# Optimization experiments

Hardware: AMD Instinct MI355X
Metric: run time of the kernel (lower is better)

Reference implementation:

```python
import jax, jax.numpy as jnp
import numpy as np

TEMPERATURE = 0.8
TOP_K = 50
TOP_P = 0.9
REP_PENALTY = 1.2
FILTER_VALUE = -1e9  # stands in for -inf in HF top_k_top_p_filtering (numerically identical probs)

B, S, V = 16, 64, 50257
P = 64  # previously generated tokens per sequence


def setup_inputs() -> dict:
    key = jax.random.key(0)
    k1, k2 = jax.random.split(key)
    logits = jax.random.normal(k1, (B, S, V), dtype=jnp.float32) * 3.0
    prev_tokens = jax.random.randint(k2, (S, P), 0, V)
    return {"logits": logits, "prev_tokens": prev_tokens}


def _repetition_penalty(logits, prev_tokens):
    # logits: [B,S,V], prev_tokens: [S,P]
    gathered = jnp.take_along_axis(logits, prev_tokens[None, :, :], axis=-1)  # [B,S,P]
    all_neg = jnp.all(gathered < 0, axis=0, keepdims=True)                    # [1,S,P]
    penalized = jnp.where(all_neg, gathered * REP_PENALTY, gathered / REP_PENALTY)
    s_idx = jnp.broadcast_to(jnp.arange(S)[:, None], prev_tokens.shape)       # [S,P]
    # scatter back (duplicate indices write identical values -> matches set() semantics)
    return logits.at[:, s_idx, prev_tokens].set(penalized)


def _top_k_top_p_filter(logits):
    # top-k: mask everything below the k-th largest logit
    if TOP_K > 0:
        kth = jax.lax.top_k(logits, TOP_K)[0][..., -1:]                       # [B,S,1]
        logits = jnp.where(logits < kth, FILTER_VALUE, logits)
    # top-p (nucleus): sort descending, mask tokens past cumulative prob TOP_P
    if TOP_P < 1.0:
        sort_idx = jnp.argsort(-logits, axis=-1)                              # [B,S,V]
        sorted_logits = jnp.take_along_axis(logits, sort_idx, axis=-1)
        cum_probs = jnp.cumsum(jax.nn.softmax(sorted_logits, axis=-1), axis=-1)
        remove_sorted = cum_probs > TOP_P
        # shift right so the first token exceeding the threshold is kept
        remove_sorted = jnp.concatenate(
            [jnp.zeros_like(remove_sorted[..., :1]), remove_sorted[..., :-1]], axis=-1)
        inv_idx = jnp.argsort(sort_idx, axis=-1)
        remove = jnp.take_along_axis(remove_sorted, inv_idx, axis=-1)
        logits = jnp.where(remove, FILTER_VALUE, logits)
    return logits


def reference(logits, prev_tokens):
    if REP_PENALTY != 1.0:
        logits = _repetition_penalty(logits, prev_tokens)
    logits = logits / TEMPERATURE
    logits = _top_k_top_p_filter(logits)
    # Categorical(logits=...) normalizes logits; return normalized log-probs
    return jax.nn.log_softmax(logits, axis=-1)
```

## Files before the change

kernel.cpp:

```cpp
#include <hip/hip_runtime.h>
#include <cstdint>
#include <cfloat>
#include <math.h>

#define BB 16
#define SS 64
#define VV 50257
#define PP 64

#define NT 1024
#define HNT 512
#define NBLK 512
#define BINS 2048
#define CAP 1536
#define BMW 1572
#define KCAP 128
#define BCAP 512
#define TRAW 6.0f

typedef float f32x4 __attribute__((ext_vector_type(4)));

__device__ __forceinline__ uint32_t fkey(float f) {
    uint32_t u = __float_as_uint(f);
    return u ^ ((uint32_t)((int32_t)u >> 31) | 0x80000000u);
}
__device__ __forceinline__ float key2f(uint32_t u) {
    uint32_t b = (u & 0x80000000u) ? (u ^ 0x80000000u) : ~u;
    return __uint_as_float(b);
}

__global__ __launch_bounds__(NT)
void sch_kernel(const float* __restrict__ logits,
                const int* __restrict__ prev,
                float* __restrict__ out)
{
    const int g   = blockIdx.x;
    const int rA  = g;
    const int rB  = g + NBLK;
    const int s   = g % SS;
    const int bA  = rA / SS;
    const int bB  = rB / SS;
    const int tid = threadIdx.x;
    const float* rowA  = logits + (size_t)rA * VV;
    const float* rowB  = logits + (size_t)rB * VV;
    float*       orowA = out    + (size_t)rA * VV;
    float*       orowB = out    + (size_t)rB * VV;

    __shared__ uint32_t s_bm[BMW];
    __shared__ float    s_cv[CAP];
    __shared__ int      s_ci[CAP];
    __shared__ float    s_cv2[CAP];
    __shared__ int      s_ci2[CAP];
    __shared__ uint32_t s_hist[BINS];
    __shared__ uint32_t s_scan[16];
    __shared__ int      s_ptok[PP];
    __shared__ int      s_pneg[PP];
    __shared__ float    s_prawA[PP];
    __shared__ float    s_prawB[PP];
    __shared__ float    s_ppenA[PP];
    __shared__ float    s_ppenB[PP];
    __shared__ float    s_binv[BCAP];
    __shared__ double   s_v64[KCAP];
    __shared__ double   s_e64[KCAP];
    __shared__ int      s_ki[KCAP];
    __shared__ float    s_kof[KCAP];
    __shared__ int      s_kiA[KCAP];
    __shared__ float    s_kofA[KCAP];
    __shared__ int    s_cnt, s_cnt2, s_cntinv, s_b50, s_need, s_cntb, s_k50, s_kp, s_Kk;
    __shared__ int    s_hbar;
    __shared__ float  s_kth, s_rc;
    __shared__ double s_lse;

    for (int i = tid; i < BMW; i += NT) s_bm[i] = 0u;
    if (tid < PP) s_pneg[tid] = 1;
    if (tid == 0) { s_cnt = 0; s_cnt2 = 0; s_cntinv = 0; s_hbar = 0; }
    __syncthreads();
    for (int pair = tid; pair < PP * BB; pair += NT) {
        int ti = pair & (PP - 1);
        int b2 = pair >> 6;
        int tok = prev[s * PP + ti];
        float gg = logits[((size_t)b2 * SS + s) * (size_t)VV + tok];
        if (gg >= 0.f) atomicAnd(&s_pneg[ti], 0);
        if (b2 == 0)  s_ptok[ti]  = tok;
        if (b2 == bA) s_prawA[ti] = gg;
        if (b2 == bB) s_prawB[ti] = gg;
    }
    __syncthreads();
    if (tid < PP) {
        int neg = s_pneg[tid];
        float ga = s_prawA[tid], gb = s_prawB[tid];
        s_ppenA[tid] = neg ? (ga * 1.2f) : (ga / 1.2f);
        s_ppenB[tid] = neg ? (gb * 1.2f) : (gb / 1.2f);
        int tok = s_ptok[tid];
        atomicOr(&s_bm[tok >> 5], 1u << (tok & 31));
    }
    __syncthreads();

    int hb_phase = 0;
    auto halfbar = [&]() {
        __threadfence_block();
        if ((tid & 63) == 0) atomicAdd(&s_hbar, 1);
        ++hb_phase;
        while (*(volatile int*)&s_hbar < 8 * hb_phase)
            __builtin_amdgcn_s_sleep(1);
        __threadfence_block();
    };

    auto kbit = [&](int t) -> uint32_t {
        return (s_bm[t >> 5] >> (t & 31)) & 1u;
    };
    auto addRawP = [&](int t, float raw, float* cv, int* ci, int* pcnt) {
        if (raw >= TRAW) {
            int pos = atomicAdd(pcnt, 1);
            if (pos < CAP) { cv[pos] = raw; ci[pos] = t; }
        }
    };
    auto streamFastP = [&](const float* row_, float* cv, int* ci, int* pcnt,
                           int t0, int nthr) {
        const int mis   = (int)(((size_t)row_ >> 2) & 3);
        const int head  = (4 - mis) & 3;
        const int nq    = (VV - head) >> 2;
        const int ttail = head + (nq << 2);
        const float4* p4 = reinterpret_cast<const float4*>(row_ + head);
        for (int t = t0; t < head; t += nthr) addRawP(t, row_[t], cv, ci, pcnt);
        int base = 0;
        for (; base + 4 * nthr <= nq; base += 4 * nthr) {
            float4 f[4];
            #pragma unroll
            for (int u = 0; u < 4; ++u) f[u] = p4[base + t0 + u * nthr];
            #pragma unroll
            for (int u = 0; u < 4; ++u) {
                int t = head + ((base + t0 + u * nthr) << 2);
                addRawP(t + 0, f[u].x, cv, ci, pcnt);
                addRawP(t + 1, f[u].y, cv, ci, pcnt);
                addRawP(t + 2, f[u].z, cv, ci, pcnt);
                addRawP(t + 3, f[u].w, cv, ci, pcnt);
            }
        }
        for (int q = base + t0; q < nq; q += nthr) {
            float4 f = p4[q];
            int t = head + (q << 2);
            addRawP(t + 0, f.x, cv, ci, pcnt);
            addRawP(t + 1, f.y, cv, ci, pcnt);
            addRawP(t + 2, f.z, cv, ci, pcnt);
            addRawP(t + 3, f.w, cv, ci, pcnt);
        }
        for (int t = ttail + t0; t < VV; t += nthr) addRawP(t, row_[t], cv, ci, pcnt);
    };
    auto ntFill = [&](float* orow_, float rc_, int t0, int nthr) {
        const int omis   = (int)(((size_t)orow_ >> 2) & 3);
        const int ohead  = (4 - omis) & 3;
        const int onq    = (VV - ohead) >> 2;
        const int ottail = ohead + (onq << 2);
        f32x4* o4 = reinterpret_cast<f32x4*>(orow_ + ohead);
        f32x4 rc4; rc4.x = rc_; rc4.y = rc_; rc4.z = rc_; rc4.w = rc_;
        for (int t = t0; t < ohead; t += nthr)
            __builtin_nontemporal_store(rc_, &orow_[t]);
        for (int q = t0; q < onq; q += nthr)
            __builtin_nontemporal_store(rc4, &o4[q]);
        for (int t = ottail + t0; t < VV; t += nthr)
            __builtin_nontemporal_store(rc_, &orow_[t]);
    };

    auto procFullH = [&](int t, float raw, bool doHist, float thr, const float* ppenS,
                         float* cv, int* ci, int* pcnt) {
        float v = raw;
        if (kbit(t)) {
            #pragma unroll 1
            for (int j = 0; j < PP; ++j)
                if (s_ptok[j] == t) { v = ppenS[j]; break; }
        }
        if (!doHist) {
            if (v >= thr) {
                int pos = atomicAdd(pcnt, 1);
                if (pos < CAP) { cv[pos] = v; ci[pos] = t; }
            }
        } else {
            atomicAdd(&s_hist[fkey(v) >> 21], 1u);
        }
    };
    auto streamFullH = [&](bool doHist, float thr, const float* row_, const float* ppenS,
                           float* cv, int* ci, int* pcnt) {
        const int mis   = (int)(((size_t)row_ >> 2) & 3);
        const int head  = (4 - mis) & 3;
        const int nq    = (VV - head) >> 2;
        const int ttail = head + (nq << 2);
        const float4* p4 = reinterpret_cast<const float4*>(row_ + head);
        for (int t = tid; t < head; t += HNT) procFullH(t, row_[t], doHist, thr, ppenS, cv, ci, pcnt);
        for (int q = tid; q < nq; q += HNT) {
            float4 f = p4[q];
            int t = head + (q << 2);
            procFullH(t + 0, f.x, doHist, thr, ppenS, cv, ci, pcnt);
            procFullH(t + 1, f.y, doHist, thr, ppenS, cv, ci, pcnt);
            procFullH(t + 2, f.z, doHist, thr, ppenS, cv, ci, pcnt);
            procFullH(t + 3, f.w, doHist, thr, ppenS, cv, ci, pcnt);
        }
        for (int t = ttail + tid; t < VV; t += HNT) procFullH(t, row_[t], doHist, thr, ppenS, cv, ci, pcnt);
    };
    auto findB50H = [&](int target) {
        halfbar();
        const int per = BINS / HNT;
        int base = tid * per;
        uint32_t loc = 0;
        #pragma unroll
        for (int k2 = 0; k2 < per; ++k2) loc += s_hist[base + k2];
        uint32_t incl = loc;
        #pragma unroll
        for (int off = 1; off < 64; off <<= 1) {
            uint32_t u = (uint32_t)__shfl_up((int)incl, off, 64);
            if ((tid & 63) >= off) incl += u;
        }
        int wid = tid >> 6;
        if ((tid & 63) == 63) s_scan[wid] = incl;
        halfbar();
        if (tid < 8) {
            uint32_t p = 0;
            for (int w = 0; w < tid; ++w) p += s_scan[w];
            s_scan[8 + tid] = p;
        }
        halfbar();
        uint32_t pre_incl = s_scan[8 + wid] + incl;
        uint32_t total    = s_scan[8 + 7] + s_scan[7];
        uint32_t run = total - pre_incl;
        for (int k2 = per - 1; k2 >= 0; --k2) {
            uint32_t h = s_hist[base + k2];
            uint32_t run2 = run + h;
            if (run < (uint32_t)target && run2 >= (uint32_t)target) {
                s_b50 = base + k2;
                s_need = target - (int)run;
            }
            run = run2;
        }
        halfbar();
    };
    auto doFallbackH = [&](const float* row_, const float* ppenS,
                           float* cv, int* ci, int* pcnt) {
        for (int i = tid; i < BINS; i += HNT) s_hist[i] = 0u;
        halfbar();
        streamFullH(true, 0.f, row_, ppenS, cv, ci, pcnt);
        findB50H(50);
        float thrF = key2f((uint32_t)s_b50 << 21);
        if (tid == 0) *pcnt = 0;
        halfbar();
        streamFullH(false, thrF, row_, ppenS, cv, ci, pcnt);
        halfbar();
    };
    auto computeKthH = [&](float* cv, int* pcnt) {
        for (int i = tid; i < BINS; i += HNT) s_hist[i] = 0u;
        if (tid == 0) { s_cntb = 0; s_kth = -FLT_MAX; }
        halfbar();
        int cc = min(*pcnt, CAP);
        for (int i = tid; i < cc; i += HNT)
            atomicAdd(&s_hist[fkey(cv[i]) >> 21], 1u);
        findB50H(50);
        int b50 = s_b50, need = s_need;
        for (int i = tid; i < cc; i += HNT) {
            if ((int)(fkey(cv[i]) >> 21) == b50) {
                int p = atomicAdd(&s_cntb, 1);
                if (p < BCAP) s_binv[p] = cv[i];
            }
        }
        halfbar();
        int cb = min(s_cntb, BCAP);
        for (int i = tid; i < cb; i += HNT) {
            float vi = s_binv[i];
            int gt = 0, ge = 0;
            for (int j = 0; j < cb; ++j) {
                float vj = s_binv[j];
                gt += (vj > vi);
                ge += (vj >= vi);
            }
            if (gt < need && ge >= need) s_kth = vi;
        }
        halfbar();
    };
    auto midPhasesH = [&](const float* row_, const float* prawS, const float* ppenS,
                          float* cv, int* ci, int* pcnt) {
        const int cntRaw = min(*pcnt, CAP);
        for (int i = tid; i < cntRaw; i += HNT) {
            if (kbit(ci[i])) {
                cv[i] = -FLT_MAX;
                atomicAdd(&s_cntinv, 1);
            }
        }
        halfbar();
        if (tid < PP) {
            int tok = s_ptok[tid];
            bool first = true;
            for (int j = 0; j < tid; ++j)
                if (s_ptok[j] == tok) { first = false; break; }
            if (first) {
                int pos = atomicAdd(pcnt, 1);
                if (pos < CAP) { cv[pos] = ppenS[tid]; ci[pos] = tok; }
            }
        }
        halfbar();
        bool fellback = false;
        {
            bool okc = (*pcnt <= CAP) && ((cntRaw - s_cntinv) >= 50);
            if (!okc) { doFallbackH(row_, ppenS, cv, ci, pcnt); fellback = true; }
        }
        computeKthH(cv, pcnt);
        if (!fellback && (s_kth - 1e-4f < TRAW)) {
            doFallbackH(row_, ppenS, cv, ci, pcnt);
            computeKthH(cv, pcnt);
        }
        if (tid == 0) s_k50 = 0;
        halfbar();
        const float gthr = s_kth - 1e-4f;
        const int cntc = min(*pcnt, CAP);
        for (int i = tid; i < cntc; i += HNT) {
            if (cv[i] >= gthr) {
                int p = atomicAdd(&s_k50, 1);
                if (p < KCAP) {
                    int tok = ci[i];
                    double v64;
                    if (kbit(tok)) {
                        int pj = 0;
                        #pragma unroll 1
                        for (int j = 0; j < PP; ++j)
                            if (s_ptok[j] == tok) { pj = j; break; }
                        double gd = (double)prawS[pj];
                        double pen = s_pneg[pj] ? (gd * 1.2) : (gd / 1.2);
                        v64 = pen / 0.8;
                    } else {
                        v64 = (double)cv[i] / 0.8;
                    }
                    s_v64[p] = v64;
                    s_ki[p]  = tok;
                }
            }
        }
        halfbar();
        const int k50c = min(s_k50, KCAP);
        for (int i = k50c + tid; i < KCAP; i += HNT) {
            s_v64[i] = -1e300;
            s_ki[i]  = (1 << 30) + i;
        }
        halfbar();
        if (tid < 64) {
            int l = tid;
            double v0 = s_v64[l],    v1 = s_v64[l + 64];
            int    i0 = s_ki[l],     i1 = s_ki[l + 64];
            for (int k = 2; k <= KCAP; k <<= 1) {
                for (int j = k >> 1; j > 0; j >>= 1) {
                    if (j >= 64) {
                        bool before = (v0 > v1) || (v0 == v1 && i0 < i1);
                        if (!before) {
                            double tv = v0; v0 = v1; v1 = tv;
                            int    ti = i0; i0 = i1; i1 = ti;
                        }
                    } else {
                        double nv0 = __shfl_xor(v0, j, 64);
                        double nv1 = __shfl_xor(v1, j, 64);
                        int    ni0 = __shfl_xor(i0, j, 64);
                        int    ni1 = __shfl_xor(i1, j, 64);
                        bool lower = ((l & j) == 0);
                        bool up0 = ((l & k) == 0);
                        bool up1 = (((l + 64) & k) == 0);
                        bool bm0 = (v0 > nv0) || (v0 == nv0 && i0 < ni0);
                        bool bm1 = (v1 > nv1) || (v1 == nv1 && i1 < ni1);
                        bool keep0 = lower ? (up0 == bm0) : (up0 != bm0);
                        bool keep1 = lower ? (up1 == bm1) : (up1 != bm1);
                        if (!keep0) { v0 = nv0; i0 = ni0; }
                        if (!keep1) { v1 = nv1; i1 = ni1; }
                    }
                }
            }
            s_v64[l] = v0; s_v64[l + 64] = v1;
            s_ki[l]  = i0; s_ki[l + 64]  = i1;
        }
        halfbar();
        if (tid == 0) {
            int kk = k50c;
            int Kkept;
            if (kk <= 50) Kkept = kk;
            else {
                double kth64 = s_v64[49];
                Kkept = 50;
                while (Kkept < kk && s_v64[Kkept] == kth64) ++Kkept;
            }
            s_Kk = Kkept;
        }
        halfbar();
        const int Kk = s_Kk;
        const double mx = s_v64[0];
        if (tid < Kk) s_e64[tid] = exp(s_v64[tid] - mx);
        halfbar();
        if (tid == 0) {
            double D = 0.0;
            #pragma unroll 1
            for (int i = 0; i < Kk; ++i) D += s_e64[i];
            double c = 0.0;
            int Kp = 0;
            #pragma unroll 1
            for (int i = 0; i < Kk; ++i) {
                bool keep = (i == 0) || (c <= 0.9);
                c += s_e64[i] / D;
                if (keep) Kp = i + 1; else break;
            }
            double D2 = 0.0;
            #pragma unroll 1
            for (int i = 0; i < Kp; ++i) D2 += s_e64[i];
            double lse = log(D2);
            s_lse = lse;
            s_rc = (float)((-1e9 - mx) - lse);
            s_kp = Kp;
        }
        halfbar();
        if (tid < s_kp) s_kof[tid] = (float)((s_v64[tid] - mx) - s_lse);
        halfbar();
    };

    streamFastP(rowA, s_cv, s_ci, &s_cnt, tid, NT);
    __syncthreads();

    if (tid < HNT) {
        midPhasesH(rowA, s_prawA, s_ppenA, s_cv, s_ci, &s_cnt);
    } else {
        streamFastP(rowB, s_cv2, s_ci2, &s_cnt2, tid - HNT, HNT);
    }
    __syncthreads();

    const float rcA = s_rc;
    const int   kpA = s_kp;
    if (tid < KCAP) { s_kiA[tid] = s_ki[tid]; s_kofA[tid] = s_kof[tid]; }
    if (tid == 0) s_cntinv = 0;
    __syncthreads();

    if (tid < HNT) {
        midPhasesH(rowB, s_prawB, s_ppenB, s_cv2, s_ci2, &s_cnt2);
    } else {
        ntFill(orowA, rcA, tid - HNT, HNT);
    }
    __syncthreads();

    if (tid < kpA) orowA[s_kiA[tid]] = s_kofA[tid];
    const float rcB = s_rc;
    ntFill(orowB, rcB, tid, NT);
    __syncthreads();
    if (tid < s_kp) orowB[s_ki[tid]] = s_kof[tid];
}

extern "C" void kernel_launch(void* const* d_in, const int* in_sizes, int n_in,
                              void* d_out, int out_size, void* d_ws, size_t ws_size,
                              hipStream_t stream) {
    const float* logits = (const float*)d_in[0];
    const int*   prev   = (const int*)d_in[1];
    float*       out    = (float*)d_out;
    dim3 grid(NBLK), block(NT);
    hipLaunchKernelGGL(sch_kernel, grid, block, 0, stream, logits, prev, out);
}
```

Baseline: 89.99 us.

## Shrink mid-phase group and work-steal row streaming and fills via shared atomic queue

Cuts the group of threads running the serial mid-phase selection (histogram, top-k, top-p) from 512 to 256. The streaming of row B and the output fills are switched to wave-level work stealing through a shared-memory atomic chunk counter. Waves that finish the mid phase early join the streaming or fill work, so the latency of the mid phase overlaps better with memory traffic. The cost is fewer threads doing the histogram and candidate work, plus extra atomics and dynamic chunk handling.

```diff
diff --git a/kernel.cpp b/kernel.cpp
--- a/kernel.cpp
+++ b/kernel.cpp
@@ -9,7 +9,8 @@
 #define PP 64
 
 #define NT 1024
-#define HNT 512
+#define HNT 256
+#define NWH (HNT / 64)
 #define NBLK 512
 #define BINS 2048
 #define CAP 1536
@@ -17,6 +18,7 @@
 #define KCAP 128
 #define BCAP 512
 #define TRAW 6.0f
+#define CHUNKQ 256
 
 typedef float f32x4 __attribute__((ext_vector_type(4)));
 
@@ -52,7 +54,7 @@
     __shared__ float    s_cv2[CAP];
     __shared__ int      s_ci2[CAP];
     __shared__ uint32_t s_hist[BINS];
-    __shared__ uint32_t s_scan[16];
+    __shared__ uint32_t s_scan[2 * NWH];
     __shared__ int      s_ptok[PP];
     __shared__ int      s_pneg[PP];
     __shared__ float    s_prawA[PP];
@@ -68,12 +70,16 @@
     __shared__ float    s_kofA[KCAP];
     __shared__ int    s_cnt, s_cnt2, s_cntinv, s_b50, s_need, s_cntb, s_k50, s_kp, s_Kk;
     __shared__ int    s_hbar;
+    __shared__ int    s_wqB, s_wqFA, s_wqFB;
     __shared__ float  s_kth, s_rc;
     __shared__ double s_lse;
 
     for (int i = tid; i < BMW; i += NT) s_bm[i] = 0u;
     if (tid < PP) s_pneg[tid] = 1;
-    if (tid == 0) { s_cnt = 0; s_cnt2 = 0; s_cntinv = 0; s_hbar = 0; }
+    if (tid == 0) {
+        s_cnt = 0; s_cnt2 = 0; s_cntinv = 0; s_hbar = 0;
+        s_wqB = 0; s_wqFA = 0; s_wqFB = 0;
+    }
     __syncthreads();
     for (int pair = tid; pair < PP * BB; pair += NT) {
         int ti = pair & (PP - 1);
@@ -101,7 +107,7 @@
         __threadfence_block();
         if ((tid & 63) == 0) atomicAdd(&s_hbar, 1);
         ++hb_phase;
-        while (*(volatile int*)&s_hbar < 8 * hb_phase)
+        while (*(volatile int*)&s_hbar < NWH * hb_phase)
             __builtin_amdgcn_s_sleep(1);
         __threadfence_block();
     };
@@ -147,19 +153,83 @@
         }
         for (int t = ttail + t0; t < VV; t += nthr) addRawP(t, row_[t], cv, ci, pcnt);
     };
-    auto ntFill = [&](float* orow_, float rc_, int t0, int nthr) {
+    auto streamWS = [&](const float* row_, float* cv, int* ci, int* pcnt, int* wq) {
+        const int mis   = (int)(((size_t)row_ >> 2) & 3);
+        const int head  = (4 - mis) & 3;
+        const int nq    = (VV - head) >> 2;
+        const int ttail = head + (nq << 2);
+        const float4* p4 = reinterpret_cast<const float4*>(row_ + head);
+        const int lane = tid & 63;
+        while (true) {
+            int c = 0;
+            if (lane == 0) c = atomicAdd(wq, 1);
+            c = __shfl(c, 0, 64);
+            if (c == 0) {
+                for (int t = lane; t < head; t += 64) addRawP(t, row_[t], cv, ci, pcnt);
+                for (int t = ttail + lane; t < VV; t += 64) addRawP(t, row_[t], cv, ci, pcnt);
+            }
+            int q0 = c * CHUNKQ;
+            if (q0 >= nq) break;
+            if (q0 + CHUNKQ <= nq) {
+                float4 f[4];
+                #pragma unroll
+                for (int u = 0; u < 4; ++u) f[u] = p4[q0 + lane + (u << 6)];
+                #pragma unroll
+                for (int u = 0; u < 4; ++u) {
+                    int t = head + ((q0 + lane + (u << 6)) << 2);
+                    addRawP(t + 0, f[u].x, cv, ci, pcnt);
+                    addRawP(t + 1, f[u].y, cv, ci, pcnt);
+                    addRawP(t + 2, f[u].z, cv, ci, pcnt);
+                    addRawP(t + 3, f[u].w, cv, ci, pcnt);
+                }
+            } else {
+                #pragma unroll
+                for (int u = 0; u < 4; ++u) {
+                    int q = q0 + lane + (u << 6);
+                    if (q < nq) {
+                        float4 f = p4[q];
+                        int t = head + (q << 2);
+                        addRawP(t + 0, f.x, cv, ci, pcnt);
+                        addRawP(t + 1, f.y, cv, ci, pcnt);
+                        addRawP(t + 2, f.z, cv, ci, pcnt);
+                        addRawP(t + 3, f.w, cv, ci, pcnt);
+                    }
+                }
+            }
+        }
+    };
+    auto ntFillWS = [&](float* orow_, float rc_, int* wq) {
         const int omis   = (int)(((size_t)orow_ >> 2) & 3);
         const int ohead  = (4 - omis) & 3;
         const int onq    = (VV - ohead) >> 2;
         const int ottail = ohead + (onq << 2);
         f32x4* o4 = reinterpret_cast<f32x4*>(orow_ + ohead);
         f32x4 rc4; rc4.x = rc_; rc4.y = rc_; rc4.z = rc_; rc4.w = rc_;
-        for (int t = t0; t < ohead; t += nthr)
-            __builtin_nontemporal_store(rc_, &orow_[t]);
-        for (int q = t0; q < onq; q += nthr)
-            __builtin_nontemporal_store(rc4, &o4[q]);
-        for (int t = ottail + t0; t < VV; t += nthr)
-            __builtin_nontemporal_store(rc_, &orow_[t]);
+        const int lane = tid & 63;
+        while (true) {
+            int c = 0;
+            if (lane == 0) c = atomicAdd(wq, 1);
+            c = __shfl(c, 0, 64);
+            if (c == 0) {
+                for (int t = lane; t < ohead; t += 64)
+                    __builtin_nontemporal_store(rc_, &orow_[t]);
+                for (int t = ottail + lane; t < VV; t += 64)
+                    __builtin_nontemporal_store(rc_, &orow_[t]);
+            }
+            int q0 = c * CHUNKQ;
+            if (q0 >= onq) break;
+            if (q0 + CHUNKQ <= onq) {
+                #pragma unroll
+                for (int u = 0; u < 4; ++u)
+                    __builtin_nontemporal_store(rc4, &o4[q0 + lane + (u << 6)]);
+            } else {
+                #pragma unroll
+                for (int u = 0; u < 4; ++u) {
+                    int q = q0 + lane + (u << 6);
+                    if (q < onq) __builtin_nontemporal_store(rc4, &o4[q]);
+                }
+            }
+        }
     };
 
     auto procFullH = [&](int t, float raw, bool doHist, float thr, const float* ppenS,
@@ -213,14 +283,14 @@
         int wid = tid >> 6;
         if ((tid & 63) == 63) s_scan[wid] = incl;
         halfbar();
-        if (tid < 8) {
+        if (tid < NWH) {
             uint32_t p = 0;
             for (int w = 0; w < tid; ++w) p += s_scan[w];
-            s_scan[8 + tid] = p;
-        }
-        halfbar();
-        uint32_t pre_incl = s_scan[8 + wid] + incl;
-        uint32_t total    = s_scan[8 + 7] + s_scan[7];
+            s_scan[NWH + tid] = p;
+        }
+        halfbar();
+        uint32_t pre_incl = s_scan[NWH + wid] + incl;
+        uint32_t total    = s_scan[NWH + NWH - 1] + s_scan[NWH - 1];
         uint32_t run = total - pre_incl;
         for (int k2 = per - 1; k2 >= 0; --k2) {
             uint32_t h = s_hist[base + k2];
@@ -417,9 +487,8 @@
 
     if (tid < HNT) {
         midPhasesH(rowA, s_prawA, s_ppenA, s_cv, s_ci, &s_cnt);
-    } else {
-        streamFastP(rowB, s_cv2, s_ci2, &s_cnt2, tid - HNT, HNT);
     }
+    streamWS(rowB, s_cv2, s_ci2, &s_cnt2, &s_wqB);
     __syncthreads();
 
     const float rcA = s_rc;
@@ -430,14 +499,13 @@
 
     if (tid < HNT) {
         midPhasesH(rowB, s_prawB, s_ppenB, s_cv2, s_ci2, &s_cnt2);
-    } else {
-        ntFill(orowA, rcA, tid - HNT, HNT);
     }
+    ntFillWS(orowA, rcA, &s_wqFA);
     __syncthreads();
 
     if (tid < kpA) orowA[s_kiA[tid]] = s_kofA[tid];
     const float rcB = s_rc;
-    ntFill(orowB, rcB, tid, NT);
+    ntFillWS(orowB, rcB, &s_wqFB);
     __syncthreads();
     if (tid < s_kp) orowB[s_ki[tid]] = s_kof[tid];
 }
```

New measurement: 126.1 us. +40.1%, slower.

## Rebalance warp-specialized split: fewer selection threads, share tail streaming work

Applied to the files above, without the earlier changes.

Shrinks the group running the selection and top-p phases from 512 to 256 threads and gives the other 768 threads the streaming side. The streaming group now takes only 13/16 of the next row's scan and of the previous row's output fill. The selection group handles the remaining 3/16 once its own phases finish. The aim is to even out the two concurrent halves so neither waits at the block barrier. The risk is that the selection phases, including the full-row histogram fallback, run slower with half as many threads.

```diff
diff --git a/kernel.cpp b/kernel.cpp
--- a/kernel.cpp
+++ b/kernel.cpp
@@ -9,7 +9,9 @@
 #define PP 64
 
 #define NT 1024
-#define HNT 512
+#define HNT 256
+#define NWH (HNT / 64)
+#define SNT (NT - HNT)
 #define NBLK 512
 #define BINS 2048
 #define CAP 1536
@@ -52,7 +54,7 @@
     __shared__ float    s_cv2[CAP];
     __shared__ int      s_ci2[CAP];
     __shared__ uint32_t s_hist[BINS];
-    __shared__ uint32_t s_scan[16];
+    __shared__ uint32_t s_scan[2 * NWH];
     __shared__ int      s_ptok[PP];
     __shared__ int      s_pneg[PP];
     __shared__ float    s_prawA[PP];
@@ -101,7 +103,7 @@
         __threadfence_block();
         if ((tid & 63) == 0) atomicAdd(&s_hbar, 1);
         ++hb_phase;
-        while (*(volatile int*)&s_hbar < 8 * hb_phase)
+        while (*(volatile int*)&s_hbar < NWH * hb_phase)
             __builtin_amdgcn_s_sleep(1);
         __threadfence_block();
     };
@@ -115,16 +117,24 @@
             if (pos < CAP) { cv[pos] = raw; ci[pos] = t; }
         }
     };
-    auto streamFastP = [&](const float* row_, float* cv, int* ci, int* pcnt,
-                           int t0, int nthr) {
+    auto geomNq = [&](const void* p) -> int {
+        int mis = (int)(((size_t)p >> 2) & 3);
+        int head = (4 - mis) & 3;
+        return (VV - head) >> 2;
+    };
+    auto streamSeg = [&](const float* row_, float* cv, int* ci, int* pcnt,
+                         int qlo, int qhi, int t0, int nthr, bool doHT) {
         const int mis   = (int)(((size_t)row_ >> 2) & 3);
         const int head  = (4 - mis) & 3;
         const int nq    = (VV - head) >> 2;
         const int ttail = head + (nq << 2);
         const float4* p4 = reinterpret_cast<const float4*>(row_ + head);
-        for (int t = t0; t < head; t += nthr) addRawP(t, row_[t], cv, ci, pcnt);
-        int base = 0;
-        for (; base + 4 * nthr <= nq; base += 4 * nthr) {
+        if (doHT) {
+            for (int t = t0; t < head; t += nthr) addRawP(t, row_[t], cv, ci, pcnt);
+            for (int t = ttail + t0; t < VV; t += nthr) addRawP(t, row_[t], cv, ci, pcnt);
+        }
+        int base = qlo;
+        for (; base + 4 * nthr <= qhi; base += 4 * nthr) {
             float4 f[4];
             #pragma unroll
             for (int u = 0; u < 4; ++u) f[u] = p4[base + t0 + u * nthr];
@@ -137,7 +147,7 @@
                 addRawP(t + 3, f[u].w, cv, ci, pcnt);
             }
         }
-        for (int q = base + t0; q < nq; q += nthr) {
+        for (int q = base + t0; q < qhi; q += nthr) {
             float4 f = p4[q];
             int t = head + (q << 2);
             addRawP(t + 0, f.x, cv, ci, pcnt);
@@ -145,21 +155,23 @@
             addRawP(t + 2, f.z, cv, ci, pcnt);
             addRawP(t + 3, f.w, cv, ci, pcnt);
         }
-        for (int t = ttail + t0; t < VV; t += nthr) addRawP(t, row_[t], cv, ci, pcnt);
-    };
-    auto ntFill = [&](float* orow_, float rc_, int t0, int nthr) {
+    };
+    auto fillSeg = [&](float* orow_, float rc_, int qlo, int qhi,
+                       int t0, int nthr, bool doHT) {
         const int omis   = (int)(((size_t)orow_ >> 2) & 3);
         const int ohead  = (4 - omis) & 3;
         const int onq    = (VV - ohead) >> 2;
         const int ottail = ohead + (onq << 2);
         f32x4* o4 = reinterpret_cast<f32x4*>(orow_ + ohead);
         f32x4 rc4; rc4.x = rc_; rc4.y = rc_; rc4.z = rc_; rc4.w = rc_;
-        for (int t = t0; t < ohead; t += nthr)
-            __builtin_nontemporal_store(rc_, &orow_[t]);
-        for (int q = t0; q < onq; q += nthr)
+        if (doHT) {
+            for (int t = t0; t < ohead; t += nthr)
+                __builtin_nontemporal_store(rc_, &orow_[t]);
+            for (int t = ottail + t0; t < VV; t += nthr)
+                __builtin_nontemporal_store(rc_, &orow_[t]);
+        }
+        for (int q = qlo + t0; q < qhi; q += nthr)
             __builtin_nontemporal_store(rc4, &o4[q]);
-        for (int t = ottail + t0; t < VV; t += nthr)
-            __builtin_nontemporal_store(rc_, &orow_[t]);
     };
 
     auto procFullH = [&](int t, float raw, bool doHist, float thr, const float* ppenS,
@@ -213,14 +225,14 @@
         int wid = tid >> 6;
         if ((tid & 63) == 63) s_scan[wid] = incl;
         halfbar();
-        if (tid < 8) {
+        if (tid < NWH) {
             uint32_t p = 0;
             for (int w = 0; w < tid; ++w) p += s_scan[w];
-            s_scan[8 + tid] = p;
-        }
-        halfbar();
-        uint32_t pre_incl = s_scan[8 + wid] + incl;
-        uint32_t total    = s_scan[8 + 7] + s_scan[7];
+            s_scan[NWH + tid] = p;
+        }
+        halfbar();
+        uint32_t pre_incl = s_scan[NWH + wid] + incl;
+        uint32_t total    = s_scan[NWH + NWH - 1] + s_scan[NWH - 1];
         uint32_t run = total - pre_incl;
         for (int k2 = per - 1; k2 >= 0; --k2) {
             uint32_t h = s_hist[base + k2];
@@ -412,13 +424,19 @@
         halfbar();
     };
 
-    streamFastP(rowA, s_cv, s_ci, &s_cnt, tid, NT);
+    const int nqB   = geomNq(rowB);
+    const int q1B   = (nqB * 13) >> 4;
+    const int onqA  = geomNq(orowA);
+    const int q1A   = (onqA * 13) >> 4;
+
+    streamSeg(rowA, s_cv, s_ci, &s_cnt, 0, geomNq(rowA), tid, NT, true);
     __syncthreads();
 
     if (tid < HNT) {
         midPhasesH(rowA, s_prawA, s_ppenA, s_cv, s_ci, &s_cnt);
+        streamSeg(rowB, s_cv2, s_ci2, &s_cnt2, q1B, nqB, tid, HNT, false);
     } else {
-        streamFastP(rowB, s_cv2, s_ci2, &s_cnt2, tid - HNT, HNT);
+        streamSeg(rowB, s_cv2, s_ci2, &s_cnt2, 0, q1B, tid - HNT, SNT, true);
     }
     __syncthreads();
 
@@ -430,14 +448,15 @@
 
     if (tid < HNT) {
         midPhasesH(rowB, s_prawB, s_ppenB, s_cv2, s_ci2, &s_cnt2);
+        fillSeg(orowA, rcA, q1A, onqA, tid, HNT, false);
     } else {
-        ntFill(orowA, rcA, tid - HNT, HNT);
+        fillSeg(orowA, rcA, 0, q1A, tid - HNT, SNT, true);
     }
     __syncthreads();
 
     if (tid < kpA) orowA[s_kiA[tid]] = s_kofA[tid];
     const float rcB = s_rc;
-    ntFill(orowB, rcB, tid, NT);
+    fillSeg(orowB, rcB, 0, geomNq(orowB), tid, NT, true);
     __syncthreads();
     if (tid < s_kp) orowB[s_ki[tid]] = s_kof[tid];
 }
```

Result: slower. 134.0 us (+48.9%).
